# Kernel optimization log

Hardware: AMD Instinct MI355X
Metric: run time of the kernel (lower is better)

## Reference

```python
import jax, jax.numpy as jnp
import numpy as np

N_BITS = 3        # routing dims (slice_mask = first 3 indices)
N_HEADS = 8       # 2**N_BITS
D_FEAT = 512      # input_dim - N_BITS
D_BASE = 1024     # base MLP output
D_HEAD_H = 1024   # head hidden
D_OUT = 512       # head output
BATCH = 8192


def setup_inputs() -> dict:
    key = jax.random.key(0)
    ks = jax.random.split(key, 8)
    s = lambda fan_in: 1.0 / np.sqrt(fan_in)
    x = jax.random.normal(ks[0], (BATCH, N_BITS + D_FEAT), dtype=jnp.float32)
    Wb = jax.random.normal(ks[1], (D_FEAT, D_BASE), dtype=jnp.float32) * s(D_FEAT)
    bb = jax.random.normal(ks[2], (D_BASE,), dtype=jnp.float32) * s(D_FEAT)
    Wh1 = jax.random.normal(ks[3], (N_HEADS, D_BASE, D_HEAD_H), dtype=jnp.float32) * s(D_BASE)
    bh1 = jax.random.normal(ks[4], (N_HEADS, D_HEAD_H), dtype=jnp.float32) * s(D_BASE)
    Wh2 = jax.random.normal(ks[5], (N_HEADS, D_HEAD_H, D_OUT), dtype=jnp.float32) * s(D_HEAD_H)
    bh2 = jax.random.normal(ks[6], (N_HEADS, D_OUT), dtype=jnp.float32) * s(D_HEAD_H)
    return {"x": x, "Wb": Wb, "bb": bb, "Wh1": Wh1, "bh1": bh1, "Wh2": Wh2, "bh2": bh2}


def _combs():
    # Faithful to the torch `recursive` construction for three single-index
    # binary slices: combs[bit, head] = (head >> bit) & 1
    return ((jnp.arange(N_HEADS)[None, :] >> jnp.arange(N_BITS)[:, None]) & 1).astype(bool)


def reference(x, Wb, bb, Wh1, bh1, Wh2, bh2):
    bits = x[:, :N_BITS] > 0.5          # [B, 3] routing bits
    feat = x[:, N_BITS:]                # [B, 512]
    base = jax.nn.relu(feat @ Wb + bb)  # [B, 1024] shared base net
    # all heads run over the full batch (as in the original module)
    h = jax.nn.relu(jnp.einsum('bd,hde->bhe', base, Wh1) + bh1[None])  # [B, 8, 1024]
    out_all = jnp.einsum('bhe,heo->bho', h, Wh2) + bh2[None]           # [B, 8, 512]
    combs = _combs()                                                   # [3, 8]
    sel = jnp.all(bits[:, :, None] == combs[None], axis=1).astype(x.dtype)  # [B, 8] one-hot
    return jnp.einsum('bho,bh->bo', out_all, sel)                      # [B, 512]
```

## Files before the change

### kernel.cpp

```cpp
#include <hip/hip_runtime.h>
#include <hip/hip_bf16.h>
#include <stdint.h>

using short8 = __attribute__((ext_vector_type(8))) short;
using f32x4  = __attribute__((ext_vector_type(4))) float;

#define NBITS 3
#define NHEADS 8
#define BATCH 8192
#define DFEAT 512
#define DBASE 1024
#define DHH   1024
#define DOUT  512
#define XCOLS (NBITS + DFEAT)

static __device__ __forceinline__ unsigned short f2bf(float f) {
    union { float f; unsigned u; } v; v.f = f;
    unsigned r = v.u + 0x7FFFu + ((v.u >> 16) & 1u);
    return (unsigned short)(r >> 16);
}

__global__ void k_bucket(const float* __restrict__ x, int* __restrict__ cnt,
                         int* __restrict__ rows) {
    int r = blockIdx.x * 256 + threadIdx.x;
    if (r >= BATCH) return;
    const float* xr = x + (size_t)r * XCOLS;
    int h = (xr[0] > 0.5f ? 1 : 0) | (xr[1] > 0.5f ? 2 : 0) | (xr[2] > 0.5f ? 4 : 0);
    int slot = atomicAdd(cnt + h, 1);
    rows[h * BATCH + slot] = r;
}

__global__ void k_feat(const float* __restrict__ x, unsigned short* __restrict__ feat) {
    int t = blockIdx.x * 256 + threadIdx.x;
    int row = t >> 6, c8 = (t & 63) << 3;
    const float* src = x + (size_t)row * XCOLS + NBITS + c8;
    short8 v;
#pragma unroll
    for (int i = 0; i < 8; ++i) v[i] = (short)f2bf(src[i]);
    *(short8*)(feat + (size_t)row * DFEAT + c8) = v;
}

__global__ void k_transpose(const float* __restrict__ W, unsigned short* __restrict__ WT,
                            int K, int N) {
    __shared__ float tile[32][33];
    int b  = blockIdx.z;
    int n0 = blockIdx.x << 5, k0 = blockIdx.y << 5;
    int tx = threadIdx.x & 31, ty = threadIdx.x >> 5;
    const float* Wb = W + (size_t)b * K * N;
    unsigned short* WTb = WT + (size_t)b * K * N;
#pragma unroll
    for (int j = 0; j < 32; j += 8)
        tile[ty + j][tx] = Wb[(size_t)(k0 + ty + j) * N + n0 + tx];
    __syncthreads();
#pragma unroll
    for (int j = 0; j < 32; j += 8)
        WTb[(size_t)(n0 + ty + j) * K + k0 + tx] = f2bf(tile[tx][ty + j]);
}

template<bool GATHER, bool RELU, bool OUTBF16>
__global__ __launch_bounds__(512, 1)
void k_gemm2(const unsigned short* __restrict__ A, int lda, int K,
             const unsigned short* __restrict__ BT,
             const float* __restrict__ bias,
             void* __restrict__ C, int ldc,
             const int* __restrict__ rowsAll, const int* __restrict__ cntAll,
             int Nfull, int nshift) {
    const int bid  = blockIdx.x;
    const int mt   = bid & 63;
    const int nt   = (bid >> 6) & ((1 << nshift) - 1);
    const int head = GATHER ? (bid >> (6 + nshift)) : 0;
    const int m0 = mt * 128;
    const int n0 = nt * 256;
    int M = BATCH;
    const int* rows = nullptr;
    if (GATHER) {
        M = cntAll[head];
        if (m0 >= M) return;
        rows = rowsAll + head * BATCH;
    }
    const unsigned short* BTh = BT + (size_t)head * Nfull * K;
    const float* biash = bias + (size_t)head * Nfull;

    __shared__ __align__(16) char lds[98304];
    char* ldsp = lds;

    const int t    = threadIdx.x;
    const int w    = t >> 6;
    const int lane = t & 63;
    const int wr = w >> 2, wc = w & 3;
    const int ln = lane & 15, lq = lane >> 4;

    const unsigned short* gA[2];
    {
        int rl  = t >> 3;
        int kch = (t & 7) ^ (rl & 7);
#pragma unroll
        for (int h = 0; h < 2; ++h) {
            int idx = m0 + h * 64 + rl;
            int r;
            if (GATHER) { idx = idx < M ? idx : (M - 1); r = rows[idx]; }
            else r = idx;
            gA[h] = A + (size_t)r * lda + kch * 8;
        }
    }
    const unsigned short* gB[2][2];
#pragma unroll
    for (int hb = 0; hb < 2; ++hb)
#pragma unroll
        for (int i = 0; i < 2; ++i) {
            int c   = i * 512 + t;
            int cl  = c >> 3;
            int kch = (c & 7) ^ (cl & 7);
            int ncol = n0 + hb * 128 + cl;
            gB[hb][i] = BTh + (size_t)ncol * K + kch * 8;
        }

#define STAGE_A(kt, d)                                                                     \
    { _Pragma("unroll") for (int h = 0; h < 2; ++h)                                        \
        __builtin_amdgcn_global_load_lds(                                                  \
            (const __attribute__((address_space(1))) void*)(gA[h] + (kt) * 64),            \
            (__attribute__((address_space(3))) void*)(ldsp + (d) * 16384 + h * 8192 + w * 1024), \
            16, 0, 0); }
#define STAGE_B(kt, d)                                                                     \
    { _Pragma("unroll") for (int hb = 0; hb < 2; ++hb)                                     \
      _Pragma("unroll") for (int i = 0; i < 2; ++i)                                        \
        __builtin_amdgcn_global_load_lds(                                                  \
            (const __attribute__((address_space(1))) void*)(gB[hb][i] + (kt) * 64),        \
            (__attribute__((address_space(3))) void*)(ldsp + 32768 + (d) * 32768 + hb * 16384 + i * 8192 + w * 1024), \
            16, 0, 0); }
#define LOAD_A(dst, d, ks)                                                                 \
    { _Pragma("unroll") for (int m = 0; m < 4; ++m) {                                      \
        int rA = wr * 64 + m * 16 + ln;                                                    \
        int ch = (((ks) << 2) | lq) ^ (ln & 7);                                            \
        dst[m] = *(const short8*)(ldsp + (d) * 16384 + rA * 128 + ch * 16); } }
#define LOAD_B(dst, d, ks)                                                                 \
    { _Pragma("unroll") for (int n = 0; n < 4; ++n) {                                      \
        int cB = wc * 64 + n * 16 + ln;                                                    \
        int ch = (((ks) << 2) | lq) ^ (ln & 7);                                            \
        dst[n] = *(const short8*)(ldsp + 32768 + (d) * 32768 + cB * 128 + ch * 16); } }
#define MFMA16(av, bv)                                                                     \
    { __builtin_amdgcn_s_setprio(1);                                                       \
      _Pragma("unroll") for (int m = 0; m < 4; ++m)                                        \
      _Pragma("unroll") for (int n = 0; n < 4; ++n)                                        \
        acc[m][n] = __builtin_amdgcn_mfma_f32_16x16x32_bf16(av[m], bv[n], acc[m][n], 0, 0, 0); \
      __builtin_amdgcn_s_setprio(0); }

    f32x4 acc[4][4] = {};
    short8 a0[4], b0[4], a1[4], b1[4];
    const int NT = K >> 6;

    STAGE_A(0, 0); STAGE_B(0, 0); STAGE_A(1, 1);
    __syncthreads();
    LOAD_A(a0, 0, 0); LOAD_B(b0, 0, 0);

    for (int kt = 0; kt < NT; ++kt) {
        const int d = kt & 1, o = d ^ 1;
        const int kB = (kt + 1 < NT) ? kt + 1 : NT - 1;
        const int kA = (kt + 2 < NT) ? kt + 2 : NT - 1;
        STAGE_B(kB, o);
        LOAD_A(a1, d, 1); LOAD_B(b1, d, 1);
        MFMA16(a0, b0);
        __syncthreads();
        STAGE_A(kA, d);
        LOAD_A(a0, o, 0); LOAD_B(b0, o, 0);
        MFMA16(a1, b1);
    }
#undef STAGE_A
#undef STAGE_B
#undef LOAD_A
#undef LOAD_B
#undef MFMA16

#pragma unroll
    for (int n = 0; n < 4; ++n) {
        int col = n0 + wc * 64 + n * 16 + ln;
        float bv = biash[col];
#pragma unroll
        for (int m = 0; m < 4; ++m) {
#pragma unroll
            for (int j = 0; j < 4; ++j) {
                int rt = wr * 64 + m * 16 + lq * 4 + j;
                int grow;
                if (GATHER) {
                    if (m0 + rt >= M) continue;
                    grow = rows[m0 + rt];
                } else {
                    grow = m0 + rt;
                }
                float v = acc[m][n][j] + bv;
                if (RELU) v = fmaxf(v, 0.0f);
                if (OUTBF16)
                    ((unsigned short*)C)[(size_t)grow * ldc + col] = f2bf(v);
                else
                    ((float*)C)[(size_t)grow * ldc + col] = v;
            }
        }
    }
}

extern "C" void kernel_launch(void* const* d_in, const int* in_sizes, int n_in,
                              void* d_out, int out_size, void* d_ws, size_t ws_size,
                              hipStream_t stream) {
    const float* x   = (const float*)d_in[0];
    const float* Wb  = (const float*)d_in[1];
    const float* bb  = (const float*)d_in[2];
    const float* Wh1 = (const float*)d_in[3];
    const float* bh1 = (const float*)d_in[4];
    const float* Wh2 = (const float*)d_in[5];
    const float* bh2 = (const float*)d_in[6];

    char* ws = (char*)d_ws;
    unsigned short* feat = (unsigned short*)(ws);
    unsigned short* WbT  = (unsigned short*)(ws + (8ull  << 20));
    unsigned short* Wh1T = (unsigned short*)(ws + (9ull  << 20));
    unsigned short* Wh2T = (unsigned short*)(ws + (25ull << 20));
    unsigned short* base = (unsigned short*)(ws + (33ull << 20));
    unsigned short* hbuf = (unsigned short*)(ws + (49ull << 20));
    int* rows            = (int*)(ws + (65ull << 20));
    int* cnt             = (int*)(ws + (65ull << 20) + (256ull << 10));

    hipMemsetAsync(cnt, 0, NHEADS * sizeof(int), stream);
    k_bucket<<<BATCH / 256, 256, 0, stream>>>(x, cnt, rows);
    k_feat<<<(BATCH * 64) / 256, 256, 0, stream>>>(x, feat);
    k_transpose<<<dim3(DBASE / 32, DFEAT / 32, 1), 256, 0, stream>>>(Wb, WbT, DFEAT, DBASE);
    k_transpose<<<dim3(DHH / 32, DBASE / 32, NHEADS), 256, 0, stream>>>(Wh1, Wh1T, DBASE, DHH);
    k_transpose<<<dim3(DOUT / 32, DHH / 32, NHEADS), 256, 0, stream>>>(Wh2, Wh2T, DHH, DOUT);

    k_gemm2<false, true, true><<<256, 512, 0, stream>>>(
        feat, DFEAT, DFEAT, WbT, bb, base, DBASE, nullptr, nullptr, DBASE, 2);
    k_gemm2<true, true, true><<<2048, 512, 0, stream>>>(
        base, DBASE, DBASE, Wh1T, bh1, hbuf, DHH, rows, cnt, DHH, 2);
    k_gemm2<true, false, false><<<1024, 512, 0, stream>>>(
        hbuf, DHH, DHH, Wh2T, bh2, d_out, DOUT, rows, cnt, DOUT, 1);
}
```

Before: 323.9 us.

## Use triple-buffered LDS pipeline with vmcnt waits and narrower tiles for last GEMM

```diff
diff --git a/kernel.cpp b/kernel.cpp
--- a/kernel.cpp
+++ b/kernel.cpp
@@ -57,20 +57,24 @@
         WTb[(size_t)(n0 + ty + j) * K + k0 + tx] = f2bf(tile[tx][ty + j]);
 }
 
-template<bool GATHER, bool RELU, bool OUTBF16>
+template<bool GATHER, bool RELU, bool OUTBF16, int NF>
 __global__ __launch_bounds__(512, 1)
-void k_gemm2(const unsigned short* __restrict__ A, int lda, int K,
+void k_gemm3(const unsigned short* __restrict__ A, int lda, int K,
              const unsigned short* __restrict__ BT,
              const float* __restrict__ bias,
              void* __restrict__ C, int ldc,
              const int* __restrict__ rowsAll, const int* __restrict__ cntAll,
              int Nfull, int nshift) {
+    constexpr int BN  = NF * 64;
+    constexpr int BNB = BN * 128;
+    constexpr int NB  = BNB / 8192;
+
     const int bid  = blockIdx.x;
     const int mt   = bid & 63;
     const int nt   = (bid >> 6) & ((1 << nshift) - 1);
     const int head = GATHER ? (bid >> (6 + nshift)) : 0;
     const int m0 = mt * 128;
-    const int n0 = nt * 256;
+    const int n0 = nt * BN;
     int M = BATCH;
     const int* rows = nullptr;
     if (GATHER) {
@@ -81,8 +85,9 @@
     const unsigned short* BTh = BT + (size_t)head * Nfull * K;
     const float* biash = bias + (size_t)head * Nfull;
 
-    __shared__ __align__(16) char lds[98304];
-    char* ldsp = lds;
+    __shared__ __align__(16) char lds[3 * 16384 + 3 * BNB];
+    char* ldsA = lds;
+    char* ldsB = lds + 3 * 16384;
 
     const int t    = threadIdx.x;
     const int w    = t >> 6;
@@ -103,77 +108,77 @@
             gA[h] = A + (size_t)r * lda + kch * 8;
         }
     }
-    const unsigned short* gB[2][2];
-#pragma unroll
-    for (int hb = 0; hb < 2; ++hb)
-#pragma unroll
-        for (int i = 0; i < 2; ++i) {
-            int c   = i * 512 + t;
-            int cl  = c >> 3;
-            int kch = (c & 7) ^ (cl & 7);
-            int ncol = n0 + hb * 128 + cl;
-            gB[hb][i] = BTh + (size_t)ncol * K + kch * 8;
-        }
-
-#define STAGE_A(kt, d)                                                                     \
+    const unsigned short* gB[NB];
+#pragma unroll
+    for (int i = 0; i < NB; ++i) {
+        int c   = i * 512 + t;
+        int cl  = c >> 3;
+        int kch = (c & 7) ^ (cl & 7);
+        gB[i] = BTh + (size_t)(n0 + cl) * K + kch * 8;
+    }
+
+#define STAGE(kt_, d_)                                                                     \
     { _Pragma("unroll") for (int h = 0; h < 2; ++h)                                        \
         __builtin_amdgcn_global_load_lds(                                                  \
-            (const __attribute__((address_space(1))) void*)(gA[h] + (kt) * 64),            \
-            (__attribute__((address_space(3))) void*)(ldsp + (d) * 16384 + h * 8192 + w * 1024), \
+            (const __attribute__((address_space(1))) void*)(gA[h] + (kt_) * 64),           \
+            (__attribute__((address_space(3))) void*)(ldsA + (d_) * 16384 + h * 8192 + w * 1024), \
+            16, 0, 0);                                                                     \
+      _Pragma("unroll") for (int i = 0; i < NB; ++i)                                       \
+        __builtin_amdgcn_global_load_lds(                                                  \
+            (const __attribute__((address_space(1))) void*)(gB[i] + (kt_) * 64),           \
+            (__attribute__((address_space(3))) void*)(ldsB + (d_) * BNB + i * 8192 + w * 1024), \
             16, 0, 0); }
-#define STAGE_B(kt, d)                                                                     \
-    { _Pragma("unroll") for (int hb = 0; hb < 2; ++hb)                                     \
-      _Pragma("unroll") for (int i = 0; i < 2; ++i)                                        \
-        __builtin_amdgcn_global_load_lds(                                                  \
-            (const __attribute__((address_space(1))) void*)(gB[hb][i] + (kt) * 64),        \
-            (__attribute__((address_space(3))) void*)(ldsp + 32768 + (d) * 32768 + hb * 16384 + i * 8192 + w * 1024), \
-            16, 0, 0); }
-#define LOAD_A(dst, d, ks)                                                                 \
-    { _Pragma("unroll") for (int m = 0; m < 4; ++m) {                                      \
-        int rA = wr * 64 + m * 16 + ln;                                                    \
-        int ch = (((ks) << 2) | lq) ^ (ln & 7);                                            \
-        dst[m] = *(const short8*)(ldsp + (d) * 16384 + rA * 128 + ch * 16); } }
-#define LOAD_B(dst, d, ks)                                                                 \
-    { _Pragma("unroll") for (int n = 0; n < 4; ++n) {                                      \
-        int cB = wc * 64 + n * 16 + ln;                                                    \
-        int ch = (((ks) << 2) | lq) ^ (ln & 7);                                            \
-        dst[n] = *(const short8*)(ldsp + 32768 + (d) * 32768 + cB * 128 + ch * 16); } }
-#define MFMA16(av, bv)                                                                     \
-    { __builtin_amdgcn_s_setprio(1);                                                       \
-      _Pragma("unroll") for (int m = 0; m < 4; ++m)                                        \
-      _Pragma("unroll") for (int n = 0; n < 4; ++n)                                        \
-        acc[m][n] = __builtin_amdgcn_mfma_f32_16x16x32_bf16(av[m], bv[n], acc[m][n], 0, 0, 0); \
-      __builtin_amdgcn_s_setprio(0); }
-
-    f32x4 acc[4][4] = {};
-    short8 a0[4], b0[4], a1[4], b1[4];
+
+#define WAITV_STEADY()                                                                     \
+    { if constexpr (NF == 4) asm volatile("s_waitcnt vmcnt(12)" ::: "memory");             \
+      else                   asm volatile("s_waitcnt vmcnt(8)"  ::: "memory"); }
+
+    f32x4 acc[4][NF] = {};
     const int NT = K >> 6;
 
-    STAGE_A(0, 0); STAGE_B(0, 0); STAGE_A(1, 1);
-    __syncthreads();
-    LOAD_A(a0, 0, 0); LOAD_B(b0, 0, 0);
+    STAGE(0, 0);
+    STAGE(1, 1);
 
     for (int kt = 0; kt < NT; ++kt) {
-        const int d = kt & 1, o = d ^ 1;
-        const int kB = (kt + 1 < NT) ? kt + 1 : NT - 1;
-        const int kA = (kt + 2 < NT) ? kt + 2 : NT - 1;
-        STAGE_B(kB, o);
-        LOAD_A(a1, d, 1); LOAD_B(b1, d, 1);
-        MFMA16(a0, b0);
-        __syncthreads();
-        STAGE_A(kA, d);
-        LOAD_A(a0, o, 0); LOAD_B(b0, o, 0);
-        MFMA16(a1, b1);
-    }
-#undef STAGE_A
-#undef STAGE_B
-#undef LOAD_A
-#undef LOAD_B
-#undef MFMA16
-
-#pragma unroll
-    for (int n = 0; n < 4; ++n) {
-        int col = n0 + wc * 64 + n * 16 + ln;
+        const int bc = kt % 3;
+        const int bs = (kt + 2) % 3;
+        const int ks = (kt + 2 < NT) ? kt + 2 : NT - 1;
+        STAGE(ks, bs);
+        WAITV_STEADY();
+        __builtin_amdgcn_s_barrier();
+        const char* cA = ldsA + bc * 16384;
+        const char* cB = ldsB + bc * BNB;
+#pragma unroll
+        for (int ksl = 0; ksl < 2; ++ksl) {
+            short8 af[4], bf[NF];
+#pragma unroll
+            for (int m = 0; m < 4; ++m) {
+                int rA = wr * 64 + m * 16 + ln;
+                int ch = ((ksl << 2) | lq) ^ (ln & 7);
+                af[m] = *(const short8*)(cA + rA * 128 + ch * 16);
+            }
+#pragma unroll
+            for (int n = 0; n < NF; ++n) {
+                int cBc = wc * (NF * 16) + n * 16 + ln;
+                int ch  = ((ksl << 2) | lq) ^ (ln & 7);
+                bf[n] = *(const short8*)(cB + cBc * 128 + ch * 16);
+            }
+            __builtin_amdgcn_s_setprio(1);
+#pragma unroll
+            for (int m = 0; m < 4; ++m)
+#pragma unroll
+                for (int n = 0; n < NF; ++n)
+                    acc[m][n] = __builtin_amdgcn_mfma_f32_16x16x32_bf16(af[m], bf[n], acc[m][n], 0, 0, 0);
+            __builtin_amdgcn_s_setprio(0);
+        }
+        __builtin_amdgcn_s_barrier();
+    }
+#undef STAGE
+#undef WAITV_STEADY
+
+#pragma unroll
+    for (int n = 0; n < NF; ++n) {
+        int col = n0 + wc * (NF * 16) + n * 16 + ln;
         float bv = biash[col];
 #pragma unroll
         for (int m = 0; m < 4; ++m) {
@@ -226,10 +231,10 @@
     k_transpose<<<dim3(DHH / 32, DBASE / 32, NHEADS), 256, 0, stream>>>(Wh1, Wh1T, DBASE, DHH);
     k_transpose<<<dim3(DOUT / 32, DHH / 32, NHEADS), 256, 0, stream>>>(Wh2, Wh2T, DHH, DOUT);
 
-    k_gemm2<false, true, true><<<256, 512, 0, stream>>>(
+    k_gemm3<false, true, true, 4><<<256, 512, 0, stream>>>(
         feat, DFEAT, DFEAT, WbT, bb, base, DBASE, nullptr, nullptr, DBASE, 2);
-    k_gemm2<true, true, true><<<2048, 512, 0, stream>>>(
+    k_gemm3<true, true, true, 4><<<2048, 512, 0, stream>>>(
         base, DBASE, DBASE, Wh1T, bh1, hbuf, DHH, rows, cnt, DHH, 2);
-    k_gemm2<true, false, false><<<1024, 512, 0, stream>>>(
-        hbuf, DHH, DHH, Wh2T, bh2, d_out, DOUT, rows, cnt, DOUT, 1);
-}
+    k_gemm3<true, false, false, 2><<<2048, 512, 0, stream>>>(
+        hbuf, DHH, DHH, Wh2T, bh2, d_out, DOUT, rows, cnt, DOUT, 2);
+}
```

Measured after the change: 349.2 us. 7.8% more time.
